# Kernel tuning notes

Measured on AMD Instinct MI355X. Metric: run time of the kernel, lower is better.

## Reference

```python
import jax, jax.numpy as jnp
import numpy as np

E4M3_MAX = 448.0
M, K, N = 131072, 512, 512


def _round_to_fp8_e4m3(x):
    # Emulated round-to-nearest E4M3: 3 mantissa bits, exponent in [-7, 8]
    abs_x = jnp.abs(x)
    sign = jnp.sign(x)
    exponent = jnp.clip(jnp.floor(jnp.log2(jnp.maximum(abs_x, 2.0 ** -9))), -7.0, 8.0)
    pow2e = jnp.exp2(exponent)
    mantissa = jnp.round(abs_x / pow2e * 8.0) / 8.0  # jnp.round is half-to-even, matching torch.round
    return sign * mantissa * pow2e


def _quantize_e4m3(x, scale):
    scaled = jnp.clip(x * scale, -E4M3_MAX, E4M3_MAX)
    return _round_to_fp8_e4m3(scaled)


def _dynamic_scale(x):
    # FP8TensorMeta.compute_scale with a single amax in history: max_value / amax * 0.9
    amax = jnp.max(jnp.abs(x))
    return jnp.where(amax > 0, E4M3_MAX / amax * 0.9, 1.0)


def setup_inputs() -> dict:
    key = jax.random.key(0)
    k1, k2, k3 = jax.random.split(key, 3)
    bound = 1.0 / np.sqrt(K)  # kaiming_uniform(a=sqrt(5)) on [N,K] -> U(-1/sqrt(K), 1/sqrt(K))
    x = jax.random.normal(k1, (M, K), dtype=jnp.float32)
    weight = jax.random.uniform(k2, (N, K), dtype=jnp.float32, minval=-bound, maxval=bound)
    bias = jax.random.uniform(k3, (N,), dtype=jnp.float32, minval=-bound, maxval=bound)
    return {"x": x, "weight": weight, "bias": bias}


def reference(x, weight, bias):
    input_scale = _dynamic_scale(x)
    weight_scale = _dynamic_scale(weight)
    x_fp8 = _quantize_e4m3(x, input_scale)          # [M, K]
    w_fp8 = _quantize_e4m3(weight, weight_scale)    # [N, K]
    out = jnp.einsum("mk,nk->mn", x_fp8, w_fp8) + bias  # F.linear
    return out / (input_scale * weight_scale)
```

## Files before the change

kernel.cpp:

```cpp
#include <hip/hip_runtime.h>

typedef unsigned short u16;
typedef unsigned int u32;
typedef __attribute__((ext_vector_type(8))) short short8;
typedef __attribute__((ext_vector_type(4))) float f32x4;

__device__ __forceinline__ u16 quant_bf16(float v, float scale) {
  float sc = v * scale;
  sc = fminf(448.0f, fmaxf(-448.0f, sc));
  u32 b = __float_as_uint(sc);
  u32 sb = (b & 0x7f800000u) + 0x0A000000u;
  sb = sb < 0x46000000u ? 0x46000000u : sb;
  float mg = __uint_as_float(sb);
  float q = (fabsf(sc) + mg) - mg;
  u32 qb = __float_as_uint(q) | (b & 0x80000000u);
  return (u16)(qb >> 16);
}

__global__ void init_ws(u32* w) {
  w[0] = 0u;
  w[1] = 0u;
}

__global__ void amax_kernel(const float4* __restrict__ p, int n4, u32* __restrict__ out) {
  float m = 0.0f;
  int idx = blockIdx.x * blockDim.x + threadIdx.x;
  int stride = gridDim.x * blockDim.x;
  for (int i = idx; i < n4; i += stride) {
    float4 v = p[i];
    m = fmaxf(m, fmaxf(fmaxf(fabsf(v.x), fabsf(v.y)), fmaxf(fabsf(v.z), fabsf(v.w))));
  }
#pragma unroll
  for (int off = 32; off > 0; off >>= 1)
    m = fmaxf(m, __shfl_down(m, off, 64));
  __shared__ float sm[4];
  int wv = threadIdx.x >> 6;
  if ((threadIdx.x & 63) == 0) sm[wv] = m;
  __syncthreads();
  if (threadIdx.x == 0) {
    float mm = fmaxf(fmaxf(sm[0], sm[1]), fmaxf(sm[2], sm[3]));
    atomicMax(out, __float_as_uint(mm));
  }
}

__global__ void scales_kernel(const u32* __restrict__ am, float* __restrict__ wsf) {
  float ax = __uint_as_float(am[0]);
  float aw = __uint_as_float(am[1]);
  float sx = ax > 0.0f ? 448.0f / ax * 0.9f : 1.0f;
  float sw = aw > 0.0f ? 448.0f / aw * 0.9f : 1.0f;
  wsf[2] = sx;
  wsf[3] = sw;
  wsf[4] = 1.0f / (sx * sw);
}

__global__ void quant_w_kernel(const float4* __restrict__ w, uint2* __restrict__ wq,
                               const float* __restrict__ wsf) {
  float sw = wsf[3];
  int i = blockIdx.x * blockDim.x + threadIdx.x;
  float4 v = w[i];
  uint2 r;
  r.x = (u32)quant_bf16(v.x, sw) | ((u32)quant_bf16(v.y, sw) << 16);
  r.y = (u32)quant_bf16(v.z, sw) | ((u32)quant_bf16(v.w, sw) << 16);
  wq[i] = r;
}

__global__ void __launch_bounds__(256) gemm_kernel(const float* __restrict__ x,
                                                   const u16* __restrict__ wq,
                                                   const float* __restrict__ bias,
                                                   float* __restrict__ out,
                                                   const float* __restrict__ wsf) {
  __shared__ u16 As[128 * 32];
  __shared__ u16 Bs[128 * 32];
  const int tid = threadIdx.x;
  const int lane = tid & 63;
  const int wv = tid >> 6;
  const int quad = lane >> 4;
  const int lr = lane & 15;
  const int m0 = blockIdx.y * 128;
  const int n0 = blockIdx.x * 128;
  const float sx = wsf[2];
  const float inv = wsf[4];
  const int wm = (wv >> 1) * 64;
  const int wn = (wv & 1) * 64;
  const int xrow = tid >> 3;
  const int xcol = (tid & 7) * 4;

  f32x4 acc[4][4] = {};

  for (int kt = 0; kt < 16; ++kt) {
    __syncthreads();
#pragma unroll
    for (int i = 0; i < 2; ++i) {
      const int c = wv + i * 4;
      const int n = c * 16 + (lane >> 2);
      const u16* gp = wq + (size_t)(n0 + n) * 512 + kt * 32 + (lane & 3) * 8;
      u16* lp = &Bs[c * 512 + lane * 8];
      __builtin_amdgcn_global_load_lds((const __attribute__((address_space(1))) u32*)gp,
                                       (__attribute__((address_space(3))) u32*)lp, 16, 0, 0);
    }
#pragma unroll
    for (int s = 0; s < 4; ++s) {
      const int r = s * 32 + xrow;
      const float4 v = *(const float4*)(x + (size_t)(m0 + r) * 512 + kt * 32 + xcol);
      uint2 pk;
      pk.x = (u32)quant_bf16(v.x, sx) | ((u32)quant_bf16(v.y, sx) << 16);
      pk.y = (u32)quant_bf16(v.z, sx) | ((u32)quant_bf16(v.w, sx) << 16);
      *(uint2*)&As[r * 32 + xcol] = pk;
    }
    __syncthreads();
    short8 af[4], bf[4];
#pragma unroll
    for (int mi = 0; mi < 4; ++mi)
      af[mi] = *(const short8*)&As[(wm + mi * 16 + lr) * 32 + quad * 8];
#pragma unroll
    for (int ni = 0; ni < 4; ++ni)
      bf[ni] = *(const short8*)&Bs[(wn + ni * 16 + lr) * 32 + quad * 8];
#pragma unroll
    for (int mi = 0; mi < 4; ++mi)
#pragma unroll
      for (int ni = 0; ni < 4; ++ni)
        acc[mi][ni] = __builtin_amdgcn_mfma_f32_16x16x32_bf16(af[mi], bf[ni], acc[mi][ni], 0, 0, 0);
  }

  float bn[4];
#pragma unroll
  for (int ni = 0; ni < 4; ++ni) bn[ni] = bias[n0 + wn + ni * 16 + lr];
#pragma unroll
  for (int mi = 0; mi < 4; ++mi) {
    const int gr = m0 + wm + mi * 16 + quad * 4;
#pragma unroll
    for (int ni = 0; ni < 4; ++ni) {
      const int gc = n0 + wn + ni * 16 + lr;
#pragma unroll
      for (int j = 0; j < 4; ++j)
        out[(size_t)(gr + j) * 512 + gc] = (acc[mi][ni][j] + bn[ni]) * inv;
    }
  }
}

extern "C" void kernel_launch(void* const* d_in, const int* in_sizes, int n_in,
                              void* d_out, int out_size, void* d_ws, size_t ws_size,
                              hipStream_t stream) {
  const float* x = (const float*)d_in[0];
  const float* w = (const float*)d_in[1];
  const float* bias = (const float*)d_in[2];
  float* out = (float*)d_out;

  const int K = 512, N = 512;
  const int M = in_sizes[0] / K;

  u32* ws_u = (u32*)d_ws;
  float* ws_f = (float*)d_ws;
  u16* wq = (u16*)((char*)d_ws + 1024);

  hipLaunchKernelGGL(init_ws, dim3(1), dim3(1), 0, stream, ws_u);
  hipLaunchKernelGGL(amax_kernel, dim3(1024), dim3(256), 0, stream,
                     (const float4*)x, (M * K) / 4, ws_u + 0);
  hipLaunchKernelGGL(amax_kernel, dim3(64), dim3(256), 0, stream,
                     (const float4*)w, (N * K) / 4, ws_u + 1);
  hipLaunchKernelGGL(scales_kernel, dim3(1), dim3(1), 0, stream, ws_u, ws_f);
  hipLaunchKernelGGL(quant_w_kernel, dim3((N * K / 4) / 256), dim3(256), 0, stream,
                     (const float4*)w, (uint2*)wq, ws_f);
  hipLaunchKernelGGL(gemm_kernel, dim3(N / 128, M / 128), dim3(256), 0, stream,
                     x, wq, bias, out, ws_f);
}
```

Before: 602.4 us.

## Merge amax passes, widen GEMM N-tile to 256, remap blocks for XCD locality

Replaces the atomic amax with one merged kernel that writes per-block partial maxima for x and w, followed by a single-block reduction that also computes the scales. This removes the init kernel and one launch. The GEMM tile grows from 128x128 to 128x256, so each x tile is read and quantized twice instead of four times, at the cost of twice as many accumulators per thread under launch_bounds(256,2). A 1D grid remaps blocks so the two N-halves of the same M rows land on the same XCD, to improve L2 reuse of x.

New measurement: 555.2 us. 1.08x faster.

```diff
diff --git a/kernel.cpp b/kernel.cpp
--- a/kernel.cpp
+++ b/kernel.cpp
@@ -17,19 +17,7 @@
   return (u16)(qb >> 16);
 }
 
-__global__ void init_ws(u32* w) {
-  w[0] = 0u;
-  w[1] = 0u;
-}
-
-__global__ void amax_kernel(const float4* __restrict__ p, int n4, u32* __restrict__ out) {
-  float m = 0.0f;
-  int idx = blockIdx.x * blockDim.x + threadIdx.x;
-  int stride = gridDim.x * blockDim.x;
-  for (int i = idx; i < n4; i += stride) {
-    float4 v = p[i];
-    m = fmaxf(m, fmaxf(fmaxf(fabsf(v.x), fabsf(v.y)), fmaxf(fabsf(v.z), fabsf(v.w))));
-  }
+__device__ __forceinline__ float block_max(float m) {
 #pragma unroll
   for (int off = 32; off > 0; off >>= 1)
     m = fmaxf(m, __shfl_down(m, off, 64));
@@ -37,20 +25,48 @@
   int wv = threadIdx.x >> 6;
   if ((threadIdx.x & 63) == 0) sm[wv] = m;
   __syncthreads();
-  if (threadIdx.x == 0) {
-    float mm = fmaxf(fmaxf(sm[0], sm[1]), fmaxf(sm[2], sm[3]));
-    atomicMax(out, __float_as_uint(mm));
-  }
+  float r = fmaxf(fmaxf(sm[0], sm[1]), fmaxf(sm[2], sm[3]));
+  __syncthreads();
+  return r;
 }
 
-__global__ void scales_kernel(const u32* __restrict__ am, float* __restrict__ wsf) {
-  float ax = __uint_as_float(am[0]);
-  float aw = __uint_as_float(am[1]);
-  float sx = ax > 0.0f ? 448.0f / ax * 0.9f : 1.0f;
-  float sw = aw > 0.0f ? 448.0f / aw * 0.9f : 1.0f;
-  wsf[2] = sx;
-  wsf[3] = sw;
-  wsf[4] = 1.0f / (sx * sw);
+#define XBLOCKS 2048
+#define WBLOCKS 64
+
+__global__ void amax2_kernel(const float4* __restrict__ x, int nx4,
+                             const float4* __restrict__ w, int nw4,
+                             float* __restrict__ px, float* __restrict__ pw) {
+  int bid = blockIdx.x;
+  const float4* p;
+  int n4, b, nb;
+  float* dst;
+  if (bid < XBLOCKS) { p = x; n4 = nx4; dst = px; b = bid; nb = XBLOCKS; }
+  else { p = w; n4 = nw4; dst = pw; b = bid - XBLOCKS; nb = WBLOCKS; }
+  float m = 0.0f;
+  int stride = nb * 256;
+  for (int i = b * 256 + threadIdx.x; i < n4; i += stride) {
+    float4 v = p[i];
+    m = fmaxf(m, fmaxf(fmaxf(fabsf(v.x), fabsf(v.y)), fmaxf(fabsf(v.z), fabsf(v.w))));
+  }
+  m = block_max(m);
+  if (threadIdx.x == 0) dst[b] = m;
+}
+
+__global__ void scales_kernel(const float* __restrict__ px, const float* __restrict__ pw,
+                              float* __restrict__ wsf) {
+  int tid = threadIdx.x;
+  float mx = 0.0f;
+  for (int i = tid; i < XBLOCKS; i += 256) mx = fmaxf(mx, px[i]);
+  mx = block_max(mx);
+  float mw = tid < WBLOCKS ? pw[tid] : 0.0f;
+  mw = block_max(mw);
+  if (tid == 0) {
+    float sx = mx > 0.0f ? 448.0f / mx * 0.9f : 1.0f;
+    float sw = mw > 0.0f ? 448.0f / mw * 0.9f : 1.0f;
+    wsf[2] = sx;
+    wsf[3] = sw;
+    wsf[4] = 1.0f / (sx * sw);
+  }
 }
 
 __global__ void quant_w_kernel(const float4* __restrict__ w, uint2* __restrict__ wq,
@@ -64,33 +80,39 @@
   wq[i] = r;
 }
 
-__global__ void __launch_bounds__(256) gemm_kernel(const float* __restrict__ x,
-                                                   const u16* __restrict__ wq,
-                                                   const float* __restrict__ bias,
-                                                   float* __restrict__ out,
-                                                   const float* __restrict__ wsf) {
+__global__ void __launch_bounds__(256, 2) gemm_kernel(const float* __restrict__ x,
+                                                      const u16* __restrict__ wq,
+                                                      const float* __restrict__ bias,
+                                                      float* __restrict__ out,
+                                                      const float* __restrict__ wsf) {
   __shared__ u16 As[128 * 32];
-  __shared__ u16 Bs[128 * 32];
+  __shared__ u16 Bs[256 * 32];
   const int tid = threadIdx.x;
   const int lane = tid & 63;
   const int wv = tid >> 6;
   const int quad = lane >> 4;
   const int lr = lane & 15;
-  const int m0 = blockIdx.y * 128;
-  const int n0 = blockIdx.x * 128;
+
+  const int lin = blockIdx.x;
+  const int xcd = lin & 7;
+  const int jn = (lin >> 3) & 1;
+  const int grp = lin >> 4;
+  const int m0 = (grp * 8 + xcd) * 128;
+  const int n0 = jn * 256;
+
   const float sx = wsf[2];
   const float inv = wsf[4];
   const int wm = (wv >> 1) * 64;
-  const int wn = (wv & 1) * 64;
+  const int wn = (wv & 1) * 128;
   const int xrow = tid >> 3;
   const int xcol = (tid & 7) * 4;
 
-  f32x4 acc[4][4] = {};
+  f32x4 acc[4][8] = {};
 
   for (int kt = 0; kt < 16; ++kt) {
     __syncthreads();
 #pragma unroll
-    for (int i = 0; i < 2; ++i) {
+    for (int i = 0; i < 4; ++i) {
       const int c = wv + i * 4;
       const int n = c * 16 + (lane >> 2);
       const u16* gp = wq + (size_t)(n0 + n) * 512 + kt * 32 + (lane & 3) * 8;
@@ -108,28 +130,28 @@
       *(uint2*)&As[r * 32 + xcol] = pk;
     }
     __syncthreads();
-    short8 af[4], bf[4];
+    short8 af[4], bf[8];
 #pragma unroll
     for (int mi = 0; mi < 4; ++mi)
       af[mi] = *(const short8*)&As[(wm + mi * 16 + lr) * 32 + quad * 8];
 #pragma unroll
-    for (int ni = 0; ni < 4; ++ni)
+    for (int ni = 0; ni < 8; ++ni)
       bf[ni] = *(const short8*)&Bs[(wn + ni * 16 + lr) * 32 + quad * 8];
 #pragma unroll
     for (int mi = 0; mi < 4; ++mi)
 #pragma unroll
-      for (int ni = 0; ni < 4; ++ni)
+      for (int ni = 0; ni < 8; ++ni)
         acc[mi][ni] = __builtin_amdgcn_mfma_f32_16x16x32_bf16(af[mi], bf[ni], acc[mi][ni], 0, 0, 0);
   }
 
-  float bn[4];
+  float bn[8];
 #pragma unroll
-  for (int ni = 0; ni < 4; ++ni) bn[ni] = bias[n0 + wn + ni * 16 + lr];
+  for (int ni = 0; ni < 8; ++ni) bn[ni] = bias[n0 + wn + ni * 16 + lr];
 #pragma unroll
   for (int mi = 0; mi < 4; ++mi) {
     const int gr = m0 + wm + mi * 16 + quad * 4;
 #pragma unroll
-    for (int ni = 0; ni < 4; ++ni) {
+    for (int ni = 0; ni < 8; ++ni) {
       const int gc = n0 + wn + ni * 16 + lr;
 #pragma unroll
       for (int j = 0; j < 4; ++j)
@@ -149,18 +171,16 @@
   const int K = 512, N = 512;
   const int M = in_sizes[0] / K;
 
-  u32* ws_u = (u32*)d_ws;
   float* ws_f = (float*)d_ws;
-  u16* wq = (u16*)((char*)d_ws + 1024);
+  float* px = ws_f + 16;
+  float* pw = ws_f + 16 + XBLOCKS;
+  u16* wq = (u16*)((char*)d_ws + 16384);
 
-  hipLaunchKernelGGL(init_ws, dim3(1), dim3(1), 0, stream, ws_u);
-  hipLaunchKernelGGL(amax_kernel, dim3(1024), dim3(256), 0, stream,
-                     (const float4*)x, (M * K) / 4, ws_u + 0);
-  hipLaunchKernelGGL(amax_kernel, dim3(64), dim3(256), 0, stream,
-                     (const float4*)w, (N * K) / 4, ws_u + 1);
-  hipLaunchKernelGGL(scales_kernel, dim3(1), dim3(1), 0, stream, ws_u, ws_f);
+  hipLaunchKernelGGL(amax2_kernel, dim3(XBLOCKS + WBLOCKS), dim3(256), 0, stream,
+                     (const float4*)x, (M * K) / 4, (const float4*)w, (N * K) / 4, px, pw);
+  hipLaunchKernelGGL(scales_kernel, dim3(1), dim3(256), 0, stream, px, pw, ws_f);
   hipLaunchKernelGGL(quant_w_kernel, dim3((N * K / 4) / 256), dim3(256), 0, stream,
                      (const float4*)w, (uint2*)wq, ws_f);
-  hipLaunchKernelGGL(gemm_kernel, dim3(N / 128, M / 128), dim3(256), 0, stream,
+  hipLaunchKernelGGL(gemm_kernel, dim3((M / 128) * 2), dim3(256), 0, stream,
                      x, wq, bias, out, ws_f);
 }
```
